# Kernel tuning notes

Measured on AMD Instinct MI355X. Metric: run time of the kernel, lower is better.

Reference implementation:

```python
import jax, jax.numpy as jnp
import numpy as np

N = 100000      # nodes
E = 1600000     # edges
R = 4           # relations
F = 128         # node feature dim
EMB = 128       # embedding size
HID = 256       # hidden size
B = 1024        # number of (nest, food) queries


def setup_inputs() -> dict:
    key = jax.random.key(0)
    ks = jax.random.split(key, 12)
    s1 = 1.0 / np.sqrt(F)
    s2 = 1.0 / np.sqrt(EMB)
    sf = 1.0 / np.sqrt(2 * EMB)
    return {
        "x": jax.random.normal(ks[0], (N, F), jnp.float32),
        "edge_index": jax.random.randint(ks[1], (2, E), 0, N),
        "edge_type": jax.random.randint(ks[2], (E,), 0, R),
        "nest_idx": jax.random.randint(ks[3], (B,), 0, N),
        "food_idx": jax.random.randint(ks[4], (B,), 0, N),
        "W_rel1": jax.random.normal(ks[5], (R, F, EMB), jnp.float32) * s1,
        "W_root1": jax.random.normal(ks[6], (F, EMB), jnp.float32) * s1,
        "b1": jnp.zeros((EMB,), jnp.float32),
        "W_rel2": jax.random.normal(ks[7], (R, EMB, EMB), jnp.float32) * s2,
        "W_root2": jax.random.normal(ks[8], (EMB, EMB), jnp.float32) * s2,
        "b2": jnp.zeros((EMB,), jnp.float32),
        "W_fc": jax.random.normal(ks[9], (2 * EMB, HID), jnp.float32) * sf,
        "b_fc": jnp.zeros((HID,), jnp.float32),
    }


def rgcn_conv(x, src, dst, etype, W_rel, W_root, b):
    # Per-relation transform of all nodes: [N, R, O]
    h = jnp.einsum('nf,rfo->nro', x, W_rel)
    msgs = h[src, etype]                      # [E, O] gather per edge
    # Mean aggregation per (dst, relation), PyG RGCNConv default
    key = dst * R + etype                     # [E]
    deg = jax.ops.segment_sum(jnp.ones((E,), x.dtype), key, num_segments=N * R)
    norm = 1.0 / jnp.maximum(deg, 1.0)
    out = jax.ops.segment_sum(msgs * norm[key][:, None], dst, num_segments=N)
    return out + x @ W_root + b


def reference(x, edge_index, edge_type, nest_idx, food_idx,
              W_rel1, W_root1, b1, W_rel2, W_root2, b2, W_fc, b_fc):
    src, dst = edge_index[0], edge_index[1]
    h = jax.nn.relu(rgcn_conv(x, src, dst, edge_type, W_rel1, W_root1, b1))
    h = rgcn_conv(h, src, dst, edge_type, W_rel2, W_root2, b2)
    combined = jnp.concatenate([h[nest_idx], h[food_idx]], axis=-1)  # [B, 2*EMB]
    return jax.nn.relu(combined @ W_fc + b_fc)                        # [B, HID]
```

## Files before the change

### kernel.cpp

```cpp
#include <hip/hip_runtime.h>
#include <stdint.h>

#define NN 100000
#define NE 1600000
#define NR 4
#define NK (NN * NR)
#define FD 128
#define KA 512
#define KT 640
#define NQ 1024
#define HIDN 256

#define NB 391
#define BSH 8
#define CAPB 8192
#define EPB 2048
#define NBLK1 ((NE + EPB - 1) / EPB)
#define MPAD 100096

using u16 = unsigned short;
using u32 = unsigned int;
typedef __attribute__((ext_vector_type(8))) __bf16 bf16x8;
typedef __attribute__((ext_vector_type(4))) float f32x4;

__device__ __forceinline__ u16 f2b(float f) {
    u32 u = __builtin_bit_cast(u32, f);
    u32 r = u + 0x7FFFu + ((u >> 16) & 1u);
    return (u16)(r >> 16);
}
__device__ __forceinline__ float b2f_lo(u32 v) {
    return __builtin_bit_cast(float, v << 16);
}
__device__ __forceinline__ float b2f_hi(u32 v) {
    return __builtin_bit_cast(float, v & 0xFFFF0000u);
}
__device__ __forceinline__ u32 pack2(float a, float b) {
    return (u32)f2b(a) | ((u32)f2b(b) << 16);
}
__device__ __forceinline__ void gload_lds16(const void* g, void* l) {
    __builtin_amdgcn_global_load_lds((const __attribute__((address_space(1))) u32*)g,
                                     (__attribute__((address_space(3))) u32*)l, 16, 0, 0);
}

__global__ __launch_bounds__(256) void bucket_scatter(const int* __restrict__ ei,
                                                      const int* __restrict__ et,
                                                      int* __restrict__ bcnt,
                                                      u32* __restrict__ bpack) {
    __shared__ int hist[NB];
    __shared__ int base[NB];
    int t = threadIdx.x;
    for (int i = t; i < NB; i += 256) hist[i] = 0;
    __syncthreads();
    int e0 = blockIdx.x * EPB;
    int rank[8];
    u32 pk[8];
    int bk[8];
#pragma unroll
    for (int j = 0; j < 8; ++j) {
        int e = e0 + j * 256 + t;
        bk[j] = -1;
        if (e < NE) {
            int src = __builtin_nontemporal_load(ei + e);
            int dst = __builtin_nontemporal_load(ei + NE + e);
            int r   = __builtin_nontemporal_load(et + e);
            bk[j] = dst >> BSH;
            pk[j] = (u32)src | ((u32)r << 17) | ((u32)(dst & 255) << 19);
            rank[j] = atomicAdd(&hist[bk[j]], 1);
        }
    }
    __syncthreads();
    for (int i = t; i < NB; i += 256) {
        int h = hist[i];
        base[i] = h ? atomicAdd(&bcnt[i], h) : 0;
    }
    __syncthreads();
#pragma unroll
    for (int j = 0; j < 8; ++j)
        if (bk[j] >= 0) bpack[(size_t)bk[j] * CAPB + base[bk[j]] + rank[j]] = pk[j];
}

__global__ __launch_bounds__(512) void bucket_scan(const int* __restrict__ bcnt,
                                                   int* __restrict__ bbase,
                                                   int* __restrict__ offs4) {
    __shared__ int sm[512];
    int t = threadIdx.x;
    int v = (t < NB) ? bcnt[t] : 0;
    sm[t] = v;
    __syncthreads();
    for (int o2 = 1; o2 < 512; o2 <<= 1) {
        int n = (t >= o2) ? sm[t - o2] : 0;
        __syncthreads();
        sm[t] += n;
        __syncthreads();
    }
    if (t < NB) bbase[t] = sm[t] - v;
    if (t == 0) offs4[NK] = NE;
}

__global__ __launch_bounds__(256) void key_scatter(const int* __restrict__ bcnt,
                                                   const int* __restrict__ bbase,
                                                   const u32* __restrict__ bpack,
                                                   int* __restrict__ offs4,
                                                   int* __restrict__ spack) {
    __shared__ int hist[1024];
    __shared__ int sm[256];
    int b = blockIdx.x, t = threadIdx.x;
    int cnt = bcnt[b];
    int gbase = bbase[b];
    const u32* seg = bpack + (size_t)b * CAPB;
#pragma unroll
    for (int j = 0; j < 4; ++j) hist[t + j * 256] = 0;
    __syncthreads();
    for (int i = t; i < cnt; i += 256) {
        u32 pk = seg[i];
        atomicAdd(&hist[pk >> 17], 1);
    }
    __syncthreads();
    int t4 = t * 4;
    int h0 = hist[t4], h1 = hist[t4 + 1], h2 = hist[t4 + 2], h3 = hist[t4 + 3];
    int s = h0 + h1 + h2 + h3;
    sm[t] = s;
    __syncthreads();
    for (int o2 = 1; o2 < 256; o2 <<= 1) {
        int n = (t >= o2) ? sm[t - o2] : 0;
        __syncthreads();
        sm[t] += n;
        __syncthreads();
    }
    int e0 = gbase + sm[t] - s;
    int e1 = e0 + h0, e2 = e1 + h1, e3 = e2 + h2;
    int k0 = b << 10;
    if (k0 + t4 + 0 < NK) offs4[k0 + t4 + 0] = e0;
    if (k0 + t4 + 1 < NK) offs4[k0 + t4 + 1] = e1;
    if (k0 + t4 + 2 < NK) offs4[k0 + t4 + 2] = e2;
    if (k0 + t4 + 3 < NK) offs4[k0 + t4 + 3] = e3;
    hist[t4] = e0; hist[t4 + 1] = e1; hist[t4 + 2] = e2; hist[t4 + 3] = e3;
    __syncthreads();
    for (int i = t; i < cnt; i += 256) {
        u32 pk = seg[i];
        int pos = atomicAdd(&hist[pk >> 17], 1);
        spack[pos] = (int)(pk & 0x1FFFFu);
    }
}

__global__ __launch_bounds__(256) void cvt_bf16(const float* __restrict__ in,
                                                u16* __restrict__ outp, int n) {
    int i = blockIdx.x * 256 + threadIdx.x;
    int idx = i * 4;
    if (idx + 3 >= n) {
        for (int j = idx; j < n; ++j) outp[j] = f2b(in[j]);
        return;
    }
    float4 v = *(const float4*)(in + idx);
    u32 lo = (u32)f2b(v.x) | ((u32)f2b(v.y) << 16);
    u32 hi = (u32)f2b(v.z) | ((u32)f2b(v.w) << 16);
    *(uint2*)(outp + idx) = make_uint2(lo, hi);
}

__global__ __launch_bounds__(256) void prep_B(const float* __restrict__ Wrel,
                                              const float* __restrict__ Wroot,
                                              u16* __restrict__ Bt) {
    int i = blockIdx.x * 256 + threadIdx.x;
    if (i >= FD * KT) return;
    int k = i % KT;
    int o = i / KT;
    float v = (k < 512) ? Wrel[(size_t)k * FD + o] : Wroot[(size_t)(k - 512) * FD + o];
    Bt[i] = f2b(v);
}

__global__ __launch_bounds__(256) void agg_kernel(const int* __restrict__ offs4,
                                                  const int* __restrict__ spack,
                                                  const u32* __restrict__ fp,
                                                  u16* __restrict__ Aout,
                                                  int rows,
                                                  const int* __restrict__ nest,
                                                  const int* __restrict__ food,
                                                  int qmode,
                                                  int* __restrict__ qnodes) {
    int wid = threadIdx.x >> 6, lane = threadIdx.x & 63;
    int row = blockIdx.x * 4 + wid;
    if (row >= rows) return;
    int node;
    if (qmode) node = (row < NQ) ? nest[row] : food[row - NQ];
    else node = row;
    node = __builtin_amdgcn_readfirstlane(node);
    if (qmode && lane == 0) qnodes[row] = node;

    const int* ob = offs4 + (size_t)node * 4;
    int o0 = __builtin_amdgcn_readfirstlane(ob[0]);
    int o1 = __builtin_amdgcn_readfirstlane(ob[1]);
    int o2 = __builtin_amdgcn_readfirstlane(ob[2]);
    int o3 = __builtin_amdgcn_readfirstlane(ob[3]);
    int o4 = __builtin_amdgcn_readfirstlane(ob[4]);

    float a00 = 0, a01 = 0, a10 = 0, a11 = 0, a20 = 0, a21 = 0, a30 = 0, a31 = 0;
    int lastIdx = o4 - 1;

    for (int i = o0; i < o4; i += 8) {
        int p[8];
#pragma unroll
        for (int j = 0; j < 8; ++j) {
            int ij = i + j;
            int cl = ij <= lastIdx ? ij : lastIdx;
            int pv = spack[cl];
            p[j] = (ij <= lastIdx) ? pv : NN;
        }
        u32 v[8];
#pragma unroll
        for (int j = 0; j < 8; ++j) v[j] = fp[(size_t)p[j] * 64 + lane];
#pragma unroll
        for (int j = 0; j < 8; ++j) {
            int ij = i + j;
            float f0 = b2f_lo(v[j]);
            float f1 = b2f_hi(v[j]);
            if (ij < o1)      { a00 += f0; a01 += f1; }
            else if (ij < o2) { a10 += f0; a11 += f1; }
            else if (ij < o3) { a20 += f0; a21 += f1; }
            else              { a30 += f0; a31 += f1; }
        }
    }

    int d0 = o1 - o0, d1 = o2 - o1, d2 = o3 - o2, d3 = o4 - o3;
    float s0 = 1.0f / (float)(d0 > 1 ? d0 : 1);
    float s1 = 1.0f / (float)(d1 > 1 ? d1 : 1);
    float s2 = 1.0f / (float)(d2 > 1 ? d2 : 1);
    float s3 = 1.0f / (float)(d3 > 1 ? d3 : 1);
    u16* Ao = Aout + (size_t)row * KA + lane * 2;
    *(u32*)(Ao + 0)   = pack2(a00 * s0, a01 * s0);
    *(u32*)(Ao + 128) = pack2(a10 * s1, a11 * s1);
    *(u32*)(Ao + 256) = pack2(a20 * s2, a21 * s2);
    *(u32*)(Ao + 384) = pack2(a30 * s3, a31 * s3);
}

__global__ __launch_bounds__(256) void gemm_lds(const u16* __restrict__ A,
                                                const u16* __restrict__ rootSrc,
                                                const int* __restrict__ rootIdx,
                                                const u16* __restrict__ Bt,
                                                const float* __restrict__ bias,
                                                void* __restrict__ Cout,
                                                int M, int relu, int outBf16) {
    __shared__ u16 As[8192];
    char* lds = (char*)As;
    int tid = threadIdx.x;
    int wid = tid >> 6, lane = tid & 63;
    int wm = wid >> 1, wn = wid & 1;
    int lr = lane & 15, hi = lane >> 4;
    int row0 = blockIdx.x * 128;

    f32x4 acc[4][4];
#pragma unroll
    for (int i = 0; i < 4; ++i)
#pragma unroll
        for (int j = 0; j < 4; ++j) acc[i][j] = (f32x4){0.f, 0.f, 0.f, 0.f};

    int srow = wid * 8 + (lane >> 3);
    int sgl  = (lane & 7);

    for (int t = 0; t < 10; ++t) {
#pragma unroll
        for (int i = 0; i < 4; ++i) {
            int r = i * 32 + srow;
            int sg = sgl ^ (r & 7);
            int gr = row0 + r;
            const u16* src;
            if (t < 8) {
                src = A + (size_t)gr * KA + t * 64 + sg * 8;
            } else {
                int idx = rootIdx ? rootIdx[gr] : gr;
                src = rootSrc + (size_t)idx * FD + (t - 8) * 64 + sg * 8;
            }
            gload_lds16(src, lds + i * 4096 + wid * 1024);
        }
        bf16x8 bfr[2][4];
#pragma unroll
        for (int kk = 0; kk < 2; ++kk)
#pragma unroll
            for (int ni = 0; ni < 4; ++ni) {
                int col = wn * 64 + ni * 16 + lr;
                bfr[kk][ni] = *reinterpret_cast<const bf16x8*>(
                    Bt + (size_t)col * KT + t * 64 + kk * 32 + hi * 8);
            }
        __syncthreads();
#pragma unroll
        for (int kk = 0; kk < 2; ++kk) {
            bf16x8 afr[4];
#pragma unroll
            for (int mi = 0; mi < 4; ++mi) {
                int r = wm * 64 + mi * 16 + lr;
                int sp = (kk * 4 + hi) ^ (r & 7);
                afr[mi] = *reinterpret_cast<const bf16x8*>(lds + r * 128 + sp * 16);
            }
#pragma unroll
            for (int mi = 0; mi < 4; ++mi)
#pragma unroll
                for (int ni = 0; ni < 4; ++ni)
                    acc[mi][ni] = __builtin_amdgcn_mfma_f32_16x16x32_bf16(afr[mi], bfr[kk][ni], acc[mi][ni], 0, 0, 0);
        }
        __syncthreads();
    }

#pragma unroll
    for (int mi = 0; mi < 4; ++mi) {
#pragma unroll
        for (int ni = 0; ni < 4; ++ni) {
            int col = wn * 64 + ni * 16 + lr;
            float bv = bias[col];
#pragma unroll
            for (int rg = 0; rg < 4; ++rg) {
                int row = row0 + wm * 64 + mi * 16 + hi * 4 + rg;
                if (row < M) {
                    float v = acc[mi][ni][rg] + bv;
                    if (relu) v = fmaxf(v, 0.f);
                    if (outBf16) ((u16*)Cout)[(size_t)row * FD + col] = f2b(v);
                    else ((float*)Cout)[(size_t)row * FD + col] = v;
                }
            }
        }
    }
}

__global__ __launch_bounds__(256) void fc_kernel(const float* __restrict__ h2q,
                                                 const float* __restrict__ Wfc,
                                                 const float* __restrict__ bfc,
                                                 float* __restrict__ out) {
    __shared__ float comb[2 * FD];
    int q = blockIdx.x, t = threadIdx.x;
    if (t < FD) comb[t] = h2q[(size_t)q * FD + t];
    else comb[t] = h2q[(size_t)(NQ + q) * FD + (t - FD)];
    __syncthreads();
    float s = bfc[t];
#pragma unroll 4
    for (int k = 0; k < 2 * FD; ++k) s += comb[k] * Wfc[(size_t)k * HIDN + t];
    out[(size_t)q * HIDN + t] = fmaxf(s, 0.f);
}

extern "C" void kernel_launch(void* const* d_in, const int* in_sizes, int n_in,
                              void* d_out, int out_size, void* d_ws, size_t ws_size,
                              hipStream_t stream) {
    const float* x      = (const float*)d_in[0];
    const int*   ei     = (const int*)d_in[1];
    const int*   et     = (const int*)d_in[2];
    const int*   nest   = (const int*)d_in[3];
    const int*   food   = (const int*)d_in[4];
    const float* Wrel1  = (const float*)d_in[5];
    const float* Wroot1 = (const float*)d_in[6];
    const float* b1     = (const float*)d_in[7];
    const float* Wrel2  = (const float*)d_in[8];
    const float* Wroot2 = (const float*)d_in[9];
    const float* b2     = (const float*)d_in[10];
    const float* Wfc    = (const float*)d_in[11];
    const float* bfc    = (const float*)d_in[12];
    float* out = (float*)d_out;

    char* w = (char*)d_ws;
    size_t off = 0;
    auto take = [&](size_t b) {
        char* p = w + off;
        off += b;
        off = (off + 255) & ~(size_t)255;
        return p;
    };
    int* bcnt   = (int*)take((size_t)NB * 4);
    int* bbase  = (int*)take((size_t)NB * 4);
    int* offs4  = (int*)take(((size_t)NK + 1) * 4);
    u32* bpack  = (u32*)take((size_t)NB * CAPB * 4);
    int* spack  = (int*)take((size_t)NE * 4);
    int* qnodes = (int*)take((size_t)2 * NQ * 4);
    u16* xh     = (u16*)take((size_t)MPAD * FD * 2);
    u16* h1     = (u16*)take((size_t)MPAD * FD * 2);
    u16* Bt1    = (u16*)take((size_t)FD * KT * 2);
    u16* Bt2    = (u16*)take((size_t)FD * KT * 2);
    u16* A1     = (u16*)take((size_t)MPAD * KA * 2);
    u16* A2     = (u16*)take((size_t)2 * NQ * KA * 2);
    float* h2q  = (float*)take((size_t)2 * NQ * FD * 4);

    hipMemsetAsync(bcnt, 0, (size_t)NB * 4, stream);
    hipMemsetAsync(xh + (size_t)NN * FD, 0, FD * 2, stream);
    hipMemsetAsync(h1 + (size_t)NN * FD, 0, FD * 2, stream);
    cvt_bf16<<<((NN * FD / 4) + 255) / 256, 256, 0, stream>>>(x, xh, NN * FD);
    prep_B<<<(FD * KT + 255) / 256, 256, 0, stream>>>(Wrel1, Wroot1, Bt1);
    prep_B<<<(FD * KT + 255) / 256, 256, 0, stream>>>(Wrel2, Wroot2, Bt2);
    bucket_scatter<<<NBLK1, 256, 0, stream>>>(ei, et, bcnt, bpack);
    bucket_scan<<<1, 512, 0, stream>>>(bcnt, bbase, offs4);
    key_scatter<<<NB, 256, 0, stream>>>(bcnt, bbase, bpack, offs4, spack);

    agg_kernel<<<(NN + 3) / 4, 256, 0, stream>>>(offs4, spack, (const u32*)xh, A1,
                                                 NN, nullptr, nullptr, 0, nullptr);
    gemm_lds<<<MPAD / 128, 256, 0, stream>>>(A1, xh, nullptr, Bt1, b1,
                                             (void*)h1, NN, 1, 1);

    agg_kernel<<<(2 * NQ + 3) / 4, 256, 0, stream>>>(offs4, spack, (const u32*)h1, A2,
                                                     2 * NQ, nest, food, 1, qnodes);
    gemm_lds<<<(2 * NQ) / 128, 256, 0, stream>>>(A2, h1, qnodes, Bt2, b2,
                                                 (void*)h2q, 2 * NQ, 0, 0);
    fc_kernel<<<NQ, 256, 0, stream>>>(h2q, Wfc, bfc, out);
}
```

Before: 271.7 us.

## Fuse edge aggregation with relation GEMM per 16-node wave tile

Replaces the separate aggregation kernel and LDS-tiled GEMM with one kernel. Each wave aggregates 16 nodes two relations at a time into a swizzled LDS tile, then runs MFMA against the relation weights and adds the root term. This removes the write and re-read of the large intermediate A matrix (about 100 MB in bf16). The cost is weaker GEMM reuse: each wave reloads the weight fragments from global memory, and aggregation latency is serialized with the MFMA work inside the wave.

```diff
diff --git a/kernel.cpp b/kernel.cpp
--- a/kernel.cpp
+++ b/kernel.cpp
@@ -6,7 +6,6 @@
 #define NR 4
 #define NK (NN * NR)
 #define FD 128
-#define KA 512
 #define KT 640
 #define NQ 1024
 #define HIDN 256
@@ -16,7 +15,8 @@
 #define CAPB 8192
 #define EPB 2048
 #define NBLK1 ((NE + EPB - 1) / EPB)
-#define MPAD 100096
+#define NT1 (NN / 16)
+#define NT2 (2 * NQ / 16)
 
 using u16 = unsigned short;
 using u32 = unsigned int;
@@ -28,18 +28,10 @@
     u32 r = u + 0x7FFFu + ((u >> 16) & 1u);
     return (u16)(r >> 16);
 }
-__device__ __forceinline__ float b2f_lo(u32 v) {
-    return __builtin_bit_cast(float, v << 16);
-}
-__device__ __forceinline__ float b2f_hi(u32 v) {
-    return __builtin_bit_cast(float, v & 0xFFFF0000u);
-}
+__device__ __forceinline__ float b2f_lo(u32 v) { return __builtin_bit_cast(float, v << 16); }
+__device__ __forceinline__ float b2f_hi(u32 v) { return __builtin_bit_cast(float, v & 0xFFFF0000u); }
 __device__ __forceinline__ u32 pack2(float a, float b) {
     return (u32)f2b(a) | ((u32)f2b(b) << 16);
-}
-__device__ __forceinline__ void gload_lds16(const void* g, void* l) {
-    __builtin_amdgcn_global_load_lds((const __attribute__((address_space(1))) u32*)g,
-                                     (__attribute__((address_space(3))) u32*)l, 16, 0, 0);
 }
 
 __global__ __launch_bounds__(256) void bucket_scatter(const int* __restrict__ ei,
@@ -168,152 +160,126 @@
     Bt[i] = f2b(v);
 }
 
-__global__ __launch_bounds__(256) void agg_kernel(const int* __restrict__ offs4,
+__global__ __launch_bounds__(256) void rgcn_fused(const int* __restrict__ offs4,
                                                   const int* __restrict__ spack,
                                                   const u32* __restrict__ fp,
-                                                  u16* __restrict__ Aout,
-                                                  int rows,
+                                                  const u16* __restrict__ rootSrc,
+                                                  const u16* __restrict__ Bt,
+                                                  const float* __restrict__ bias,
+                                                  void* __restrict__ outp,
+                                                  int ntiles,
                                                   const int* __restrict__ nest,
                                                   const int* __restrict__ food,
-                                                  int qmode,
-                                                  int* __restrict__ qnodes) {
-    int wid = threadIdx.x >> 6, lane = threadIdx.x & 63;
-    int row = blockIdx.x * 4 + wid;
-    if (row >= rows) return;
-    int node;
-    if (qmode) node = (row < NQ) ? nest[row] : food[row - NQ];
-    else node = row;
-    node = __builtin_amdgcn_readfirstlane(node);
-    if (qmode && lane == 0) qnodes[row] = node;
-
-    const int* ob = offs4 + (size_t)node * 4;
-    int o0 = __builtin_amdgcn_readfirstlane(ob[0]);
-    int o1 = __builtin_amdgcn_readfirstlane(ob[1]);
-    int o2 = __builtin_amdgcn_readfirstlane(ob[2]);
-    int o3 = __builtin_amdgcn_readfirstlane(ob[3]);
-    int o4 = __builtin_amdgcn_readfirstlane(ob[4]);
-
-    float a00 = 0, a01 = 0, a10 = 0, a11 = 0, a20 = 0, a21 = 0, a30 = 0, a31 = 0;
-    int lastIdx = o4 - 1;
-
-    for (int i = o0; i < o4; i += 8) {
-        int p[8];
-#pragma unroll
-        for (int j = 0; j < 8; ++j) {
-            int ij = i + j;
-            int cl = ij <= lastIdx ? ij : lastIdx;
-            int pv = spack[cl];
-            p[j] = (ij <= lastIdx) ? pv : NN;
-        }
-        u32 v[8];
-#pragma unroll
-        for (int j = 0; j < 8; ++j) v[j] = fp[(size_t)p[j] * 64 + lane];
-#pragma unroll
-        for (int j = 0; j < 8; ++j) {
-            int ij = i + j;
-            float f0 = b2f_lo(v[j]);
-            float f1 = b2f_hi(v[j]);
-            if (ij < o1)      { a00 += f0; a01 += f1; }
-            else if (ij < o2) { a10 += f0; a11 += f1; }
-            else if (ij < o3) { a20 += f0; a21 += f1; }
-            else              { a30 += f0; a31 += f1; }
-        }
-    }
-
-    int d0 = o1 - o0, d1 = o2 - o1, d2 = o3 - o2, d3 = o4 - o3;
-    float s0 = 1.0f / (float)(d0 > 1 ? d0 : 1);
-    float s1 = 1.0f / (float)(d1 > 1 ? d1 : 1);
-    float s2 = 1.0f / (float)(d2 > 1 ? d2 : 1);
-    float s3 = 1.0f / (float)(d3 > 1 ? d3 : 1);
-    u16* Ao = Aout + (size_t)row * KA + lane * 2;
-    *(u32*)(Ao + 0)   = pack2(a00 * s0, a01 * s0);
-    *(u32*)(Ao + 128) = pack2(a10 * s1, a11 * s1);
-    *(u32*)(Ao + 256) = pack2(a20 * s2, a21 * s2);
-    *(u32*)(Ao + 384) = pack2(a30 * s3, a31 * s3);
-}
-
-__global__ __launch_bounds__(256) void gemm_lds(const u16* __restrict__ A,
-                                                const u16* __restrict__ rootSrc,
-                                                const int* __restrict__ rootIdx,
-                                                const u16* __restrict__ Bt,
-                                                const float* __restrict__ bias,
-                                                void* __restrict__ Cout,
-                                                int M, int relu, int outBf16) {
-    __shared__ u16 As[8192];
-    char* lds = (char*)As;
-    int tid = threadIdx.x;
-    int wid = tid >> 6, lane = tid & 63;
-    int wm = wid >> 1, wn = wid & 1;
+                                                  int qmode) {
+    __shared__ u16 ldsAll[4 * 16 * 256];
+    int tid = threadIdx.x, wid = tid >> 6, lane = tid & 63;
+    int tile = blockIdx.x * 4 + wid;
+    if (tile >= ntiles) return;
+    int n0 = tile * 16;
     int lr = lane & 15, hi = lane >> 4;
-    int row0 = blockIdx.x * 128;
-
-    f32x4 acc[4][4];
-#pragma unroll
-    for (int i = 0; i < 4; ++i)
-#pragma unroll
-        for (int j = 0; j < 4; ++j) acc[i][j] = (f32x4){0.f, 0.f, 0.f, 0.f};
-
-    int srow = wid * 8 + (lane >> 3);
-    int sgl  = (lane & 7);
-
-    for (int t = 0; t < 10; ++t) {
-#pragma unroll
-        for (int i = 0; i < 4; ++i) {
-            int r = i * 32 + srow;
-            int sg = sgl ^ (r & 7);
-            int gr = row0 + r;
-            const u16* src;
-            if (t < 8) {
-                src = A + (size_t)gr * KA + t * 64 + sg * 8;
+    char* L = (char*)ldsAll + wid * 8192;
+
+    f32x4 acc[8];
+#pragma unroll
+    for (int i = 0; i < 8; ++i) acc[i] = (f32x4){0.f, 0.f, 0.f, 0.f};
+
+#pragma unroll
+    for (int pass = 0; pass < 2; ++pass) {
+        for (int i = 0; i < 16; ++i) {
+            int row = n0 + i;
+            int node = qmode ? ((row < NQ) ? nest[row] : food[row - NQ]) : row;
+            node = __builtin_amdgcn_readfirstlane(node);
+            const int* ob = offs4 + (size_t)node * 4 + pass * 2;
+            int s0 = __builtin_amdgcn_readfirstlane(ob[0]);
+            int s1 = __builtin_amdgcn_readfirstlane(ob[1]);
+            int s2 = __builtin_amdgcn_readfirstlane(ob[2]);
+            float a0 = 0, a1 = 0, c0 = 0, c1 = 0;
+            {
+                int last = s1 - 1;
+                for (int e = s0; e < s1; e += 8) {
+                    int p[8];
+                    u32 v[8];
+#pragma unroll
+                    for (int j = 0; j < 8; ++j) {
+                        int ij = e + j;
+                        int cl = ij <= last ? ij : last;
+                        int pv = spack[cl];
+                        p[j] = (ij <= last) ? pv : NN;
+                    }
+#pragma unroll
+                    for (int j = 0; j < 8; ++j) v[j] = fp[(size_t)p[j] * 64 + lane];
+#pragma unroll
+                    for (int j = 0; j < 8; ++j) { a0 += b2f_lo(v[j]); a1 += b2f_hi(v[j]); }
+                }
+            }
+            {
+                int last = s2 - 1;
+                for (int e = s1; e < s2; e += 8) {
+                    int p[8];
+                    u32 v[8];
+#pragma unroll
+                    for (int j = 0; j < 8; ++j) {
+                        int ij = e + j;
+                        int cl = ij <= last ? ij : last;
+                        int pv = spack[cl];
+                        p[j] = (ij <= last) ? pv : NN;
+                    }
+#pragma unroll
+                    for (int j = 0; j < 8; ++j) v[j] = fp[(size_t)p[j] * 64 + lane];
+#pragma unroll
+                    for (int j = 0; j < 8; ++j) { c0 += b2f_lo(v[j]); c1 += b2f_hi(v[j]); }
+                }
+            }
+            int d0 = s1 - s0, d1 = s2 - s1;
+            float f0 = 1.0f / (float)(d0 > 1 ? d0 : 1);
+            float f1 = 1.0f / (float)(d1 > 1 ? d1 : 1);
+            int swz = (i & 7) << 4;
+            *(u32*)(L + i * 512 + ((lane * 4) ^ swz)) = pack2(a0 * f0, a1 * f0);
+            *(u32*)(L + i * 512 + ((256 + lane * 4) ^ swz)) = pack2(c0 * f1, c1 * f1);
+        }
+#pragma unroll
+        for (int kk = 0; kk < 8; ++kk) {
+            bf16x8 af = *reinterpret_cast<const bf16x8*>(
+                L + lr * 512 + ((kk * 64 + hi * 16) ^ ((lr & 7) << 4)));
+#pragma unroll
+            for (int nt = 0; nt < 8; ++nt) {
+                int col = nt * 16 + lr;
+                bf16x8 bfr = *reinterpret_cast<const bf16x8*>(
+                    Bt + (size_t)col * KT + pass * 256 + kk * 32 + hi * 8);
+                acc[nt] = __builtin_amdgcn_mfma_f32_16x16x32_bf16(af, bfr, acc[nt], 0, 0, 0);
+            }
+        }
+    }
+
+    {
+        int grow = n0 + lr;
+        int node = qmode ? ((grow < NQ) ? nest[grow] : food[grow - NQ]) : grow;
+        const u16* rp = rootSrc + (size_t)node * FD + hi * 8;
+#pragma unroll
+        for (int kk = 0; kk < 4; ++kk) {
+            bf16x8 af = *reinterpret_cast<const bf16x8*>(rp + kk * 32);
+#pragma unroll
+            for (int nt = 0; nt < 8; ++nt) {
+                int col = nt * 16 + lr;
+                bf16x8 bfr = *reinterpret_cast<const bf16x8*>(
+                    Bt + (size_t)col * KT + 512 + kk * 32 + hi * 8);
+                acc[nt] = __builtin_amdgcn_mfma_f32_16x16x32_bf16(af, bfr, acc[nt], 0, 0, 0);
+            }
+        }
+    }
+
+#pragma unroll
+    for (int nt = 0; nt < 8; ++nt) {
+        int col = nt * 16 + lr;
+        float bv = bias[col];
+#pragma unroll
+        for (int rg = 0; rg < 4; ++rg) {
+            int row = n0 + hi * 4 + rg;
+            float v = acc[nt][rg] + bv;
+            if (qmode) {
+                ((float*)outp)[(size_t)row * FD + col] = v;
             } else {
-                int idx = rootIdx ? rootIdx[gr] : gr;
-                src = rootSrc + (size_t)idx * FD + (t - 8) * 64 + sg * 8;
-            }
-            gload_lds16(src, lds + i * 4096 + wid * 1024);
-        }
-        bf16x8 bfr[2][4];
-#pragma unroll
-        for (int kk = 0; kk < 2; ++kk)
-#pragma unroll
-            for (int ni = 0; ni < 4; ++ni) {
-                int col = wn * 64 + ni * 16 + lr;
-                bfr[kk][ni] = *reinterpret_cast<const bf16x8*>(
-                    Bt + (size_t)col * KT + t * 64 + kk * 32 + hi * 8);
-            }
-        __syncthreads();
-#pragma unroll
-        for (int kk = 0; kk < 2; ++kk) {
-            bf16x8 afr[4];
-#pragma unroll
-            for (int mi = 0; mi < 4; ++mi) {
-                int r = wm * 64 + mi * 16 + lr;
-                int sp = (kk * 4 + hi) ^ (r & 7);
-                afr[mi] = *reinterpret_cast<const bf16x8*>(lds + r * 128 + sp * 16);
-            }
-#pragma unroll
-            for (int mi = 0; mi < 4; ++mi)
-#pragma unroll
-                for (int ni = 0; ni < 4; ++ni)
-                    acc[mi][ni] = __builtin_amdgcn_mfma_f32_16x16x32_bf16(afr[mi], bfr[kk][ni], acc[mi][ni], 0, 0, 0);
-        }
-        __syncthreads();
-    }
-
-#pragma unroll
-    for (int mi = 0; mi < 4; ++mi) {
-#pragma unroll
-        for (int ni = 0; ni < 4; ++ni) {
-            int col = wn * 64 + ni * 16 + lr;
-            float bv = bias[col];
-#pragma unroll
-            for (int rg = 0; rg < 4; ++rg) {
-                int row = row0 + wm * 64 + mi * 16 + hi * 4 + rg;
-                if (row < M) {
-                    float v = acc[mi][ni][rg] + bv;
-                    if (relu) v = fmaxf(v, 0.f);
-                    if (outBf16) ((u16*)Cout)[(size_t)row * FD + col] = f2b(v);
-                    else ((float*)Cout)[(size_t)row * FD + col] = v;
-                }
+                ((u16*)outp)[(size_t)row * FD + col] = f2b(fmaxf(v, 0.f));
             }
         }
     }
@@ -365,13 +331,10 @@
     int* offs4  = (int*)take(((size_t)NK + 1) * 4);
     u32* bpack  = (u32*)take((size_t)NB * CAPB * 4);
     int* spack  = (int*)take((size_t)NE * 4);
-    int* qnodes = (int*)take((size_t)2 * NQ * 4);
-    u16* xh     = (u16*)take((size_t)MPAD * FD * 2);
-    u16* h1     = (u16*)take((size_t)MPAD * FD * 2);
+    u16* xh     = (u16*)take((size_t)(NN + 1) * FD * 2);
+    u16* h1     = (u16*)take((size_t)(NN + 1) * FD * 2);
     u16* Bt1    = (u16*)take((size_t)FD * KT * 2);
     u16* Bt2    = (u16*)take((size_t)FD * KT * 2);
-    u16* A1     = (u16*)take((size_t)MPAD * KA * 2);
-    u16* A2     = (u16*)take((size_t)2 * NQ * KA * 2);
     float* h2q  = (float*)take((size_t)2 * NQ * FD * 4);
 
     hipMemsetAsync(bcnt, 0, (size_t)NB * 4, stream);
@@ -384,14 +347,11 @@
     bucket_scan<<<1, 512, 0, stream>>>(bcnt, bbase, offs4);
     key_scatter<<<NB, 256, 0, stream>>>(bcnt, bbase, bpack, offs4, spack);
 
-    agg_kernel<<<(NN + 3) / 4, 256, 0, stream>>>(offs4, spack, (const u32*)xh, A1,
-                                                 NN, nullptr, nullptr, 0, nullptr);
-    gemm_lds<<<MPAD / 128, 256, 0, stream>>>(A1, xh, nullptr, Bt1, b1,
-                                             (void*)h1, NN, 1, 1);
-
-    agg_kernel<<<(2 * NQ + 3) / 4, 256, 0, stream>>>(offs4, spack, (const u32*)h1, A2,
-                                                     2 * NQ, nest, food, 1, qnodes);
-    gemm_lds<<<(2 * NQ) / 128, 256, 0, stream>>>(A2, h1, qnodes, Bt2, b2,
-                                                 (void*)h2q, 2 * NQ, 0, 0);
+    rgcn_fused<<<(NT1 + 3) / 4, 256, 0, stream>>>(offs4, spack, (const u32*)xh, xh,
+                                                  Bt1, b1, (void*)h1, NT1,
+                                                  nullptr, nullptr, 0);
+    rgcn_fused<<<(NT2 + 3) / 4, 256, 0, stream>>>(offs4, spack, (const u32*)h1, h1,
+                                                  Bt2, b2, (void*)h2q, NT2,
+                                                  nest, food, 1);
     fc_kernel<<<NQ, 256, 0, stream>>>(h2q, Wfc, bfc, out);
 }
```

Result: slower. 430.9 us (+58.6%).

## Pad per-node edge lists to multiples of eight and drop global bucket scan

Applied to the files above, without the earlier changes.

The CSR layout changes so that each bucket writes into its own fixed-capacity region and each node's edge list is padded to a multiple of eight with dummy entries pointing at a zero row. Per-node offsets now hold six values including the padded end. This removes the separate single-block scan kernel and lets the aggregation loop drop its clamp and bounds logic, reading indices as wave-uniform scalars. The cost is a larger spack buffer, a serial per-thread padding fill, and an offs array with a six-int stride.

```diff
diff --git a/kernel.cpp b/kernel.cpp
--- a/kernel.cpp
+++ b/kernel.cpp
@@ -28,12 +28,8 @@
     u32 r = u + 0x7FFFu + ((u >> 16) & 1u);
     return (u16)(r >> 16);
 }
-__device__ __forceinline__ float b2f_lo(u32 v) {
-    return __builtin_bit_cast(float, v << 16);
-}
-__device__ __forceinline__ float b2f_hi(u32 v) {
-    return __builtin_bit_cast(float, v & 0xFFFF0000u);
-}
+__device__ __forceinline__ float b2f_lo(u32 v) { return __builtin_bit_cast(float, v << 16); }
+__device__ __forceinline__ float b2f_hi(u32 v) { return __builtin_bit_cast(float, v & 0xFFFF0000u); }
 __device__ __forceinline__ u32 pack2(float a, float b) {
     return (u32)f2b(a) | ((u32)f2b(b) << 16);
 }
@@ -79,47 +75,25 @@
         if (bk[j] >= 0) bpack[(size_t)bk[j] * CAPB + base[bk[j]] + rank[j]] = pk[j];
 }
 
-__global__ __launch_bounds__(512) void bucket_scan(const int* __restrict__ bcnt,
-                                                   int* __restrict__ bbase,
-                                                   int* __restrict__ offs4) {
-    __shared__ int sm[512];
-    int t = threadIdx.x;
-    int v = (t < NB) ? bcnt[t] : 0;
-    sm[t] = v;
-    __syncthreads();
-    for (int o2 = 1; o2 < 512; o2 <<= 1) {
-        int n = (t >= o2) ? sm[t - o2] : 0;
-        __syncthreads();
-        sm[t] += n;
-        __syncthreads();
-    }
-    if (t < NB) bbase[t] = sm[t] - v;
-    if (t == 0) offs4[NK] = NE;
-}
-
 __global__ __launch_bounds__(256) void key_scatter(const int* __restrict__ bcnt,
-                                                   const int* __restrict__ bbase,
                                                    const u32* __restrict__ bpack,
-                                                   int* __restrict__ offs4,
+                                                   int* __restrict__ offs6,
                                                    int* __restrict__ spack) {
     __shared__ int hist[1024];
     __shared__ int sm[256];
     int b = blockIdx.x, t = threadIdx.x;
     int cnt = bcnt[b];
-    int gbase = bbase[b];
     const u32* seg = bpack + (size_t)b * CAPB;
 #pragma unroll
     for (int j = 0; j < 4; ++j) hist[t + j * 256] = 0;
     __syncthreads();
-    for (int i = t; i < cnt; i += 256) {
-        u32 pk = seg[i];
-        atomicAdd(&hist[pk >> 17], 1);
-    }
+    for (int i = t; i < cnt; i += 256) atomicAdd(&hist[seg[i] >> 17], 1);
     __syncthreads();
     int t4 = t * 4;
     int h0 = hist[t4], h1 = hist[t4 + 1], h2 = hist[t4 + 2], h3 = hist[t4 + 3];
     int s = h0 + h1 + h2 + h3;
-    sm[t] = s;
+    int sp = (s + 7) & ~7;
+    sm[t] = sp;
     __syncthreads();
     for (int o2 = 1; o2 < 256; o2 <<= 1) {
         int n = (t >= o2) ? sm[t - o2] : 0;
@@ -127,14 +101,15 @@
         sm[t] += n;
         __syncthreads();
     }
-    int e0 = gbase + sm[t] - s;
-    int e1 = e0 + h0, e2 = e1 + h1, e3 = e2 + h2;
-    int k0 = b << 10;
-    if (k0 + t4 + 0 < NK) offs4[k0 + t4 + 0] = e0;
-    if (k0 + t4 + 1 < NK) offs4[k0 + t4 + 1] = e1;
-    if (k0 + t4 + 2 < NK) offs4[k0 + t4 + 2] = e2;
-    if (k0 + t4 + 3 < NK) offs4[k0 + t4 + 3] = e3;
+    int bas = b * CAPB + sm[t] - sp;
+    int e0 = bas, e1 = e0 + h0, e2 = e1 + h1, e3 = e2 + h2, e4 = e3 + h3, eL = bas + sp;
+    int node = (b << 8) + t;
+    if (node < NN) {
+        int* o = offs6 + (size_t)node * 6;
+        o[0] = e0; o[1] = e1; o[2] = e2; o[3] = e3; o[4] = e4; o[5] = eL;
+    }
     hist[t4] = e0; hist[t4 + 1] = e1; hist[t4 + 2] = e2; hist[t4 + 3] = e3;
+    for (int i = e4; i < eL; ++i) spack[i] = NN;
     __syncthreads();
     for (int i = t; i < cnt; i += 256) {
         u32 pk = seg[i];
@@ -168,7 +143,7 @@
     Bt[i] = f2b(v);
 }
 
-__global__ __launch_bounds__(256) void agg_kernel(const int* __restrict__ offs4,
+__global__ __launch_bounds__(256) void agg_kernel(const int* __restrict__ offs6,
                                                   const int* __restrict__ spack,
                                                   const u32* __restrict__ fp,
                                                   u16* __restrict__ Aout,
@@ -186,31 +161,27 @@
     node = __builtin_amdgcn_readfirstlane(node);
     if (qmode && lane == 0) qnodes[row] = node;
 
-    const int* ob = offs4 + (size_t)node * 4;
+    const int* ob = offs6 + (size_t)node * 6;
     int o0 = __builtin_amdgcn_readfirstlane(ob[0]);
     int o1 = __builtin_amdgcn_readfirstlane(ob[1]);
     int o2 = __builtin_amdgcn_readfirstlane(ob[2]);
     int o3 = __builtin_amdgcn_readfirstlane(ob[3]);
     int o4 = __builtin_amdgcn_readfirstlane(ob[4]);
+    int oL = __builtin_amdgcn_readfirstlane(ob[5]);
 
     float a00 = 0, a01 = 0, a10 = 0, a11 = 0, a20 = 0, a21 = 0, a30 = 0, a31 = 0;
-    int lastIdx = o4 - 1;
-
-    for (int i = o0; i < o4; i += 8) {
+
+    for (int e = o0; e < oL; e += 8) {
         int p[8];
+        u32 v[8];
+#pragma unroll
+        for (int j = 0; j < 8; ++j)
+            p[j] = __builtin_amdgcn_readfirstlane(spack[e + j]);
+#pragma unroll
+        for (int j = 0; j < 8; ++j) v[j] = fp[(size_t)p[j] * 64 + lane];
 #pragma unroll
         for (int j = 0; j < 8; ++j) {
-            int ij = i + j;
-            int cl = ij <= lastIdx ? ij : lastIdx;
-            int pv = spack[cl];
-            p[j] = (ij <= lastIdx) ? pv : NN;
-        }
-        u32 v[8];
-#pragma unroll
-        for (int j = 0; j < 8; ++j) v[j] = fp[(size_t)p[j] * 64 + lane];
-#pragma unroll
-        for (int j = 0; j < 8; ++j) {
-            int ij = i + j;
+            int ij = e + j;
             float f0 = b2f_lo(v[j]);
             float f1 = b2f_hi(v[j]);
             if (ij < o1)      { a00 += f0; a01 += f1; }
@@ -361,10 +332,9 @@
         return p;
     };
     int* bcnt   = (int*)take((size_t)NB * 4);
-    int* bbase  = (int*)take((size_t)NB * 4);
-    int* offs4  = (int*)take(((size_t)NK + 1) * 4);
+    int* offs6  = (int*)take((size_t)NN * 6 * 4);
     u32* bpack  = (u32*)take((size_t)NB * CAPB * 4);
-    int* spack  = (int*)take((size_t)NE * 4);
+    int* spack  = (int*)take((size_t)NB * CAPB * 4);
     int* qnodes = (int*)take((size_t)2 * NQ * 4);
     u16* xh     = (u16*)take((size_t)MPAD * FD * 2);
     u16* h1     = (u16*)take((size_t)MPAD * FD * 2);
@@ -381,15 +351,14 @@
     prep_B<<<(FD * KT + 255) / 256, 256, 0, stream>>>(Wrel1, Wroot1, Bt1);
     prep_B<<<(FD * KT + 255) / 256, 256, 0, stream>>>(Wrel2, Wroot2, Bt2);
     bucket_scatter<<<NBLK1, 256, 0, stream>>>(ei, et, bcnt, bpack);
-    bucket_scan<<<1, 512, 0, stream>>>(bcnt, bbase, offs4);
-    key_scatter<<<NB, 256, 0, stream>>>(bcnt, bbase, bpack, offs4, spack);
-
-    agg_kernel<<<(NN + 3) / 4, 256, 0, stream>>>(offs4, spack, (const u32*)xh, A1,
+    key_scatter<<<NB, 256, 0, stream>>>(bcnt, bpack, offs6, spack);
+
+    agg_kernel<<<(NN + 3) / 4, 256, 0, stream>>>(offs6, spack, (const u32*)xh, A1,
                                                  NN, nullptr, nullptr, 0, nullptr);
     gemm_lds<<<MPAD / 128, 256, 0, stream>>>(A1, xh, nullptr, Bt1, b1,
                                              (void*)h1, NN, 1, 1);
 
-    agg_kernel<<<(2 * NQ + 3) / 4, 256, 0, stream>>>(offs4, spack, (const u32*)h1, A2,
+    agg_kernel<<<(2 * NQ + 3) / 4, 256, 0, stream>>>(offs6, spack, (const u32*)h1, A2,
                                                      2 * NQ, nest, food, 1, qnodes);
     gemm_lds<<<(2 * NQ) / 128, 256, 0, stream>>>(A2, h1, qnodes, Bt2, b2,
                                                  (void*)h2q, 2 * NQ, 0, 0);
```

New measurement: 256.5 us. 5.6% less time.
